# Kernel optimization log

Hardware: AMD Instinct MI355X
Metric: run time of the kernel (lower is better)

The kernel has to match this reference:

```python
import jax, jax.numpy as jnp
import numpy as np

B, S, HID = 2, 4096, 1024
H, D = 16, 64

def rotate_half(x):
    x1, x2 = jnp.split(x, 2, axis=-1)
    return jnp.concatenate([-x2, x1], axis=-1)

def setup_inputs() -> dict:
    key = jax.random.key(0)
    ks = jax.random.split(key, 8)
    hidden_states = jax.random.normal(ks[0], (B, S, HID), dtype=jnp.float32)
    pos = jnp.arange(S, dtype=jnp.float32)[:, None]
    inv_freq = 1.0 / (10000.0 ** (jnp.arange(0, D, 2, dtype=jnp.float32) / D))
    freqs = pos * inv_freq[None, :]
    emb = jnp.concatenate([freqs, freqs], axis=-1)  # [S, D]
    cos = jnp.cos(emb)
    sin = jnp.sin(emb)
    W_rkv = jax.random.normal(ks[1], (3 * H * D, HID), dtype=jnp.float32) * 0.02
    W_o = jax.random.normal(ks[2], (HID, H * D), dtype=jnp.float32) * 0.02
    # match torch init: uniform(-8,-5), uniform(-1,1), uniform(0.2,0.8)
    time_decay = jax.random.uniform(ks[3], (H, D), minval=-8.0, maxval=-5.0, dtype=jnp.float32)
    time_first = jax.random.uniform(ks[4], (H, D), minval=-1.0, maxval=1.0, dtype=jnp.float32)
    time_mix = jax.random.uniform(ks[5], (1, 1, HID), minval=0.2, maxval=0.8, dtype=jnp.float32)
    return {"hidden_states": hidden_states, "cos": cos, "sin": sin,
            "W_rkv": W_rkv, "W_o": W_o, "time_decay": time_decay,
            "time_first": time_first, "time_mix": time_mix}

def reference(hidden_states, cos, sin, W_rkv, W_o, time_decay, time_first, time_mix):
    b, s, hid = hidden_states.shape
    # token-shift time mixing
    xx = jnp.concatenate([jnp.zeros_like(hidden_states[:, :1]), hidden_states[:, :-1]], axis=1)
    mixed = hidden_states * time_mix + xx * (1.0 - time_mix)
    rkv = jnp.einsum('bsh,oh->bso', mixed, W_rkv).reshape(b, s, 3, H, D)
    r = jax.nn.sigmoid(rkv[:, :, 0])  # [B,S,H,D]
    k = rkv[:, :, 1]
    v = rkv[:, :, 2]
    # rotary on r, k
    c = cos[None, :, None, :]
    sn = sin[None, :, None, :]
    r = r * c + rotate_half(r) * sn
    k = k * c + rotate_half(k) * sn
    # fast rwkv linear attention (parallel approximation)
    w = -jnp.exp(time_decay)
    kv = k * v  # [B,S,H,D]
    pos = jnp.arange(s, dtype=hidden_states.dtype)
    pos_diff = pos[:, None] - pos[None, :]  # [S,S]
    mask = pos_diff > 0  # i > j masked (per original code)
    avg_decay = jnp.mean(w)
    pd = jnp.where(mask, 0.0, pos_diff)
    dw = jnp.where(mask, 0.0, jnp.exp(avg_decay * -jnp.abs(pd)))
    dw = dw / (dw.sum(axis=1, keepdims=True) + 1e-8)
    weighted_kv = jnp.einsum('ij,bjhd->bihd', dw, kv)
    out = r * (time_first[None, None] * kv + weighted_kv)  # [B,S,H,D]
    out = out.reshape(b, s, H * D)
    return jnp.einsum('bso,ho->bsh', out, W_o)
```

## Files before the change

### kernel.cpp

```cpp
#include <hip/hip_runtime.h>
#include <math.h>

#define S_LEN 4096
#define HIDN  1024
#define NH    16
#define HD    64
#define BATCH 2
#define M_TOTAL (BATCH * S_LEN)
#define N_RKV   (3 * HIDN)
#define CS 128
#define NC (S_LEN / CS)

typedef __attribute__((ext_vector_type(8))) _Float16 f16x8;
typedef __attribute__((ext_vector_type(4))) float f32x4;
typedef __attribute__((ext_vector_type(4))) unsigned short u16x4;

__device__ __forceinline__ unsigned short f2h(float x) {
    _Float16 h = (_Float16)x;
    return *(unsigned short*)&h;
}
__device__ __forceinline__ float h2f(unsigned short b) {
    _Float16 h = *(_Float16*)&b;
    return (float)h;
}

__device__ __forceinline__ void load_lds16(const void* g, void* l) {
    __builtin_amdgcn_global_load_lds((const __attribute__((address_space(1))) void*)g,
                                     (__attribute__((address_space(3))) void*)l, 16, 0, 0);
}

__global__ void k_avg_decay(const float* __restrict__ td, float* __restrict__ a_out) {
    int t = threadIdx.x;
    double acc = 0.0;
    for (int i = t; i < NH * HD; i += 64) acc += exp((double)td[i]);
    for (int off = 32; off > 0; off >>= 1) acc += __shfl_down(acc, off, 64);
    if (t == 0) a_out[0] = (float)(acc / (double)(NH * HD));
}

__global__ __launch_bounds__(256)
void k_split_mix(const float* __restrict__ hs, const float* __restrict__ tm,
                 unsigned short* __restrict__ Ah) {
    int g = blockIdx.x * 256 + threadIdx.x;
    int kc = (g & 255) * 4;
    int m = g >> 8;
    float4 cur = *(const float4*)&hs[(size_t)m * HIDN + kc];
    float4 t4  = *(const float4*)&tm[kc];
    float4 prev = make_float4(0.f, 0.f, 0.f, 0.f);
    if (m & (S_LEN - 1)) prev = *(const float4*)&hs[(size_t)(m - 1) * HIDN + kc];
    u16x4 h;
    h.x = f2h(cur.x * t4.x + prev.x * (1.f - t4.x));
    h.y = f2h(cur.y * t4.y + prev.y * (1.f - t4.y));
    h.z = f2h(cur.z * t4.z + prev.z * (1.f - t4.z));
    h.w = f2h(cur.w * t4.w + prev.w * (1.f - t4.w));
    *(u16x4*)&Ah[(size_t)m * HIDN + kc] = h;
}

__global__ __launch_bounds__(256)
void k_split_w(const float* __restrict__ W, unsigned short* __restrict__ Wh) {
    int g = blockIdx.x * 256 + threadIdx.x;
    size_t o = (size_t)g * 4;
    float4 v = *(const float4*)&W[o];
    u16x4 h;
    h.x = f2h(v.x); h.y = f2h(v.y); h.z = f2h(v.z); h.w = f2h(v.w);
    *(u16x4*)&Wh[o] = h;
}

__device__ __forceinline__ f32x4 mfma16(f16x8 a, f16x8 b, f32x4 c) {
    return __builtin_amdgcn_mfma_f32_16x16x32_f16(a, b, c, 0, 0, 0);
}

#define SBAR  do { __builtin_amdgcn_sched_barrier(0); __builtin_amdgcn_s_barrier(); \
                   __builtin_amdgcn_sched_barrier(0); } while (0)
#define LGKM0 do { asm volatile("s_waitcnt lgkmcnt(0)" ::: "memory"); \
                   __builtin_amdgcn_sched_barrier(0); } while (0)
#define VMC(n) asm volatile("s_waitcnt vmcnt(" #n ")" ::: "memory")

__global__ __launch_bounds__(512, 2)
void k_gemm1_8ph(const unsigned short* __restrict__ A,
                 const unsigned short* __restrict__ Bm,
                 unsigned short* __restrict__ C)
{
    __shared__ unsigned short smem[57344];
    const int tid  = threadIdx.x;
    const int lane = tid & 63;
    const int wv   = tid >> 6;
    const int wm = wv >> 2, wn = wv & 3;
    const int lm = lane & 15, rq = lane >> 4;
    const int swz = (lm & 7) << 4;

    const int cpx = gridDim.x >> 3;
    const int wg  = (blockIdx.x & 7) * cpx + (blockIdx.x >> 3);
    const int bx  = wg & 15;
    const int by  = wg >> 4;
    const int m0 = by * 256, n0 = bx * 192;

    const int srow = 8 * wv + (lane >> 3);
    const int scol = ((lane & 7) ^ (lane >> 3)) * 8;
    const unsigned short* sA = A  + (size_t)(m0 + srow) * 1024 + scol;
    const unsigned short* sB = Bm + (size_t)(n0 + srow) * 1024 + scol;
    unsigned short* dA = smem + wv * 512;
    unsigned short* dB = smem + 16384 + wv * 512;

#define STG_A(u, T, bf) load_lds16(sA + (u)*65536 + (T)*64, dA + (bf)*28672 + (u)*4096)
#define STG_B(u, T, bf) load_lds16(sB + (u)*65536 + (T)*64, dB + (bf)*28672 + (u)*4096)

    const int arow = (wm * 128 + lm) * 128 + rq * 16;
    int boff[3][2];
#pragma unroll
    for (int nt = 0; nt < 3; ++nt)
#pragma unroll
        for (int kk = 0; kk < 2; ++kk)
            boff[nt][kk] = (((wn * 48 + nt * 16 + lm) * 128 + rq * 16 + kk * 64) ^ swz);

    f16x8 aF[2][2], bF[3][2];
    f32x4 acc[8][3] = {};

#define READ_A(q, bf) { const char* Ab = (const char*)smem + (bf)*57344; \
    _Pragma("unroll") for (int m2 = 0; m2 < 2; ++m2) \
    _Pragma("unroll") for (int kk = 0; kk < 2; ++kk) \
        aF[m2][kk] = *(const f16x8*)(Ab + ((arow + (q)*4096 + m2*2048 + kk*64) ^ swz)); }

#define READ_B(bf) { const char* Bb = (const char*)smem + (bf)*57344 + 32768; \
    _Pragma("unroll") for (int nt = 0; nt < 3; ++nt) \
    _Pragma("unroll") for (int kk = 0; kk < 2; ++kk) \
        bF[nt][kk] = *(const f16x8*)(Bb + boff[nt][kk]); }

#define MMQ(q) { __builtin_amdgcn_s_setprio(1); \
    _Pragma("unroll") for (int kk = 0; kk < 2; ++kk) \
    _Pragma("unroll") for (int m2 = 0; m2 < 2; ++m2) \
    _Pragma("unroll") for (int nt = 0; nt < 3; ++nt) \
        acc[(q)*2+m2][nt] = mfma16(aF[m2][kk], bF[nt][kk], acc[(q)*2+m2][nt]); \
    __builtin_amdgcn_s_setprio(0); }

    STG_A(0,0,0); STG_A(1,0,0); STG_A(2,0,0); STG_A(3,0,0);
    STG_B(0,0,0); STG_B(1,0,0); STG_B(2,0,0);
    STG_B(0,1,1); STG_B(1,1,1); STG_B(2,1,1);
    STG_A(0,1,1); STG_A(2,1,1);
    VMC(5);
    SBAR;

    for (int it = 0; it < 8; ++it) {
        const int t = 2 * it;
        const bool st = (it < 7);
        READ_A(0, 0); READ_B(0);
        STG_A(1, t + 1, 1); STG_A(3, t + 1, 1);
        SBAR; LGKM0; MMQ(0); SBAR;
        READ_A(1, 0);
        if (st) { STG_B(0, t + 2, 0); STG_B(1, t + 2, 0); }
        SBAR; LGKM0; MMQ(1); SBAR;
        READ_A(2, 0);
        if (st) { STG_B(2, t + 2, 0); STG_A(0, t + 2, 0); }
        SBAR; LGKM0; MMQ(2); SBAR;
        READ_A(3, 0);
        if (st) { STG_A(2, t + 2, 0); }
        SBAR; LGKM0; MMQ(3);
        if (st) { VMC(5); } else { VMC(0); }
        SBAR;
        READ_A(0, 1); READ_B(1);
        if (st) { STG_A(1, t + 2, 0); STG_A(3, t + 2, 0); }
        SBAR; LGKM0; MMQ(0); SBAR;
        READ_A(1, 1);
        if (st) { STG_B(0, t + 3, 1); STG_B(1, t + 3, 1); }
        SBAR; LGKM0; MMQ(1); SBAR;
        READ_A(2, 1);
        if (st) { STG_B(2, t + 3, 1); STG_A(0, t + 3, 1); }
        SBAR; LGKM0; MMQ(2); SBAR;
        READ_A(3, 1);
        if (st) { STG_A(2, t + 3, 1); }
        SBAR; LGKM0; MMQ(3);
        if (st) { VMC(5); }
        SBAR;
    }

#pragma unroll
    for (int mt = 0; mt < 8; ++mt)
#pragma unroll
        for (int nt = 0; nt < 3; ++nt) {
            int col = n0 + wn * 48 + nt * 16 + lm;
#pragma unroll
            for (int r = 0; r < 4; ++r) {
                int row = m0 + wm * 128 + mt * 16 + rq * 4 + r;
                C[(size_t)row * N_RKV + col] = f2h(acc[mt][nt][r]);
            }
        }
}

template<int LDC, int NBX, bool HALF_OUT>
__global__ __launch_bounds__(256, 2)
void k_gemm_bt(const unsigned short* __restrict__ A,
               const unsigned short* __restrict__ Bm,
               void* __restrict__ Cv)
{
    __shared__ unsigned short smem[16384];
    const int tid  = threadIdx.x;
    const int lane = tid & 63;
    const int wave = tid >> 6;
    const int wm = wave >> 1, wn = wave & 1;

    const int cpx = gridDim.x >> 3;
    const int wg  = (blockIdx.x & 7) * cpx + (blockIdx.x >> 3);
    const int bx  = wg % NBX;
    const int by  = wg / NBX;
    const int m0 = by * 128;
    const int n0 = bx * 128;

    const unsigned short* segsrc[4];
    int segdst[4];
    {
        int rowoff = lane >> 2;
        int q = (lane & 3) ^ (rowoff & 3);
#pragma unroll
        for (int i = 0; i < 4; ++i) {
            int s = wave * 4 + i;
            const unsigned short* base = (s < 8) ? A : Bm;
            int row = (s < 8) ? (m0 + s * 16) : (n0 + (s - 8) * 16);
            segsrc[i] = base + (size_t)(row + rowoff) * 1024 + q * 8;
            segdst[i] = s * 512;
        }
    }

    const int lm = lane & 15;
    const int rq = lane >> 4;
    const int qx = rq ^ (lane & 3);
    int aoff[4], boff2[4];
#pragma unroll
    for (int t = 0; t < 4; ++t) {
        aoff[t]  = (wm * 64 + t * 16 + lm) * 32 + qx * 8;
        boff2[t] = 4096 + (wn * 64 + t * 16 + lm) * 32 + qx * 8;
    }

    f32x4 acc[4][4] = {};

#pragma unroll
    for (int i = 0; i < 4; ++i) load_lds16(segsrc[i], smem + segdst[i]);

    int p = 0;
    for (int kt = 0; kt < 1024; kt += 32) {
        __syncthreads();
        if (kt + 32 < 1024) {
#pragma unroll
            for (int i = 0; i < 4; ++i)
                load_lds16(segsrc[i] + kt + 32, smem + ((p ^ 1) * 8192 + segdst[i]));
        }
        const unsigned short* sb = smem + p * 8192;
        f16x8 fah[4], fb[4];
#pragma unroll
        for (int t = 0; t < 4; ++t) {
            fah[t] = *(const f16x8*)(sb + aoff[t]);
            fb[t]  = *(const f16x8*)(sb + boff2[t]);
        }
#pragma unroll
        for (int mt = 0; mt < 4; ++mt)
#pragma unroll
            for (int nt = 0; nt < 4; ++nt)
                acc[mt][nt] = mfma16(fah[mt], fb[nt], acc[mt][nt]);
        p ^= 1;
    }

#pragma unroll
    for (int mt = 0; mt < 4; ++mt)
#pragma unroll
        for (int nt = 0; nt < 4; ++nt) {
            int col = n0 + wn * 64 + nt * 16 + lm;
#pragma unroll
            for (int r = 0; r < 4; ++r) {
                int row = m0 + wm * 64 + mt * 16 + rq * 4 + r;
                if constexpr (HALF_OUT)
                    ((unsigned short*)Cv)[(size_t)row * LDC + col] = f2h(acc[mt][nt][r]);
                else
                    ((float*)Cv)[(size_t)row * LDC + col] = acc[mt][nt][r];
            }
        }
}

__global__ __launch_bounds__(256)
void k_cb(const unsigned short* __restrict__ rkv,
          const float* __restrict__ cosp, const float* __restrict__ sinp,
          const float* __restrict__ a_ptr, float* __restrict__ Cb)
{
    __shared__ float Ls[4][64][4];
    int bid = blockIdx.x;
    int c  = bid & (NC - 1);
    int bh = bid >> 5;
    int b = bh >> 4, h = bh & 15;
    int lane = threadIdx.x & 63;
    int wave = threadIdx.x >> 6;
    int lm = lane & 15;
    int rs = lane >> 4;
    int d0 = lm * 4;
    float a = a_ptr[0];
    float sgn = (lm < 8) ? -1.f : 1.f;
    float ps0 = 0.f, ps1 = 0.f, ps2 = 0.f, ps3 = 0.f;
#pragma unroll
    for (int it = 0; it < 8; ++it) {
        int t = wave * 32 + it * 4 + rs;
        int s = c * CS + t;
        const unsigned short* rk = rkv + ((size_t)b * S_LEN + s) * N_RKV + h * 64 + d0;
        u16x4 k4 = *(const u16x4*)(rk + 1024);
        u16x4 v4 = *(const u16x4*)(rk + 2048);
        float4 cs4 = *(const float4*)&cosp[s * HD + d0];
        float4 sn4 = *(const float4*)&sinp[s * HD + d0];
        float e = expf(a * (float)t);
        float k0 = h2f(k4.x), k1 = h2f(k4.y), k2 = h2f(k4.z), k3 = h2f(k4.w);
        float kp0 = __shfl_xor(k0, 8, 64);
        float kp1 = __shfl_xor(k1, 8, 64);
        float kp2 = __shfl_xor(k2, 8, 64);
        float kp3 = __shfl_xor(k3, 8, 64);
        ps0 += e * (k0 * cs4.x + sgn * kp0 * sn4.x) * h2f(v4.x);
        ps1 += e * (k1 * cs4.y + sgn * kp1 * sn4.y) * h2f(v4.y);
        ps2 += e * (k2 * cs4.z + sgn * kp2 * sn4.z) * h2f(v4.z);
        ps3 += e * (k3 * cs4.w + sgn * kp3 * sn4.w) * h2f(v4.w);
    }
    Ls[wave][lane][0] = ps0; Ls[wave][lane][1] = ps1;
    Ls[wave][lane][2] = ps2; Ls[wave][lane][3] = ps3;
    __syncthreads();
    if (threadIdx.x < 64) {
        int d = threadIdx.x;
        int lmm = d >> 2, j = d & 3;
        float sum = 0.f;
#pragma unroll
        for (int wvv = 0; wvv < 4; ++wvv)
#pragma unroll
            for (int r = 0; r < 4; ++r)
                sum += Ls[wvv][r * 16 + lmm][j];
        Cb[((size_t)bh * NC + c) * 64 + d] = sum;
    }
}

__global__ __launch_bounds__(64)
void k_chunk_suffix(const float* __restrict__ Cb, const float* __restrict__ a_ptr,
                    float* __restrict__ Sb) {
    int bh = blockIdx.x;
    int d = threadIdx.x;
    float a = a_ptr[0];
    float eaCS = expf(a * (float)CS);
    float run = 0.f;
    Sb[(size_t)(bh * NC + NC - 1) * 64 + d] = 0.f;
    for (int c = NC - 2; c >= 0; --c) {
        run = Cb[(size_t)(bh * NC + c + 1) * 64 + d] + eaCS * run;
        Sb[(size_t)(bh * NC + c) * 64 + d] = run;
    }
}

__global__ __launch_bounds__(256)
void k_ztab(const float* __restrict__ a_ptr, float* __restrict__ Zt) {
    int i = blockIdx.x * 256 + threadIdx.x;
    if (i < S_LEN) {
        float a = a_ptr[0];
        float em1a = expm1f(a);
        Zt[i] = 1.f / (expm1f(a * (float)(S_LEN - i)) / em1a + 1e-8f);
    }
}

__global__ __launch_bounds__(256)
void k_wkv2(const unsigned short* __restrict__ rkv,
            const float* __restrict__ cosp, const float* __restrict__ sinp,
            const float* __restrict__ Sb, const float* __restrict__ a_ptr,
            const float* __restrict__ tf, const float* __restrict__ Zt,
            unsigned short* __restrict__ outH) {
    __shared__ unsigned short L[3 * 128 * 64];
    __shared__ float Tl[4][64];
    int bid = blockIdx.x;
    int c  = bid & (NC - 1);
    int bh = bid >> 5;
    int b = bh >> 4, h = bh & 15;
    int lane = threadIdx.x & 63;
    int wave = threadIdx.x >> 6;
    int s0 = c * CS;

#pragma unroll
    for (int i = 0; i < 12; ++i) {
        int seg = wave * 12 + i;
        int stream = seg >> 4;
        int rg = seg & 15;
        int row = rg * 8 + (lane >> 3);
        const unsigned short* src = rkv
            + ((size_t)b * S_LEN + s0 + row) * N_RKV + stream * 1024 + h * 64
            + (lane & 7) * 8;
        load_lds16(src, L + stream * 8192 + rg * 512);
    }
    __syncthreads();

    float a = a_ptr[0];
    float ea = expf(a);
    const unsigned short* Lr = L;
    const unsigned short* Lk = L + 8192;
    const unsigned short* Lv = L + 16384;
    float sgn = (lane < 32) ? -1.f : 1.f;
    int lx = lane ^ 32;

    float kvreg[32], rreg[32];
    float w = 1.f, T = 0.f;
#pragma unroll
    for (int t = 0; t < 32; ++t) {
        int row = wave * 32 + t;
        float r_ = h2f(Lr[row * 64 + lane]);
        float k_ = h2f(Lk[row * 64 + lane]);
        float kp = h2f(Lk[row * 64 + lx]);
        float v_ = h2f(Lv[row * 64 + lane]);
        float cs = cosp[(s0 + row) * HD + lane];
        float sn = sinp[(s0 + row) * HD + lane];
        float sig = 1.f / (1.f + expf(-r_));
        float sigp = __shfl_xor(sig, 32, 64);
        rreg[t]  = sig * cs + sgn * sigp * sn;
        kvreg[t] = (k_ * cs + sgn * kp * sn) * v_;
        T += w * kvreg[t];
        w *= ea;
    }
    Tl[wave][lane] = T;
    __syncthreads();

    float e32 = expf(a * 32.f);
    float S_run = Sb[(size_t)bid * 64 + lane] * expf(a * 32.f * (float)(3 - wave));
    float f = 1.f;
    for (int wp = wave + 1; wp < 4; ++wp) {
        S_run += f * Tl[wp][lane];
        f *= e32;
    }
    float tfv = tf[h * HD + lane];
#pragma unroll
    for (int t = 31; t >= 0; --t) {
        float kv = kvreg[t];
        S_run = kv + ea * S_run;
        int ig = s0 + wave * 32 + t;
        float o = rreg[t] * (tfv * kv + S_run * Zt[ig]);
        size_t m = (size_t)b * S_LEN + ig;
        outH[m * HIDN + h * HD + lane] = f2h(o);
    }
}

extern "C" void kernel_launch(void* const* d_in, const int* in_sizes, int n_in,
                              void* d_out, int out_size, void* d_ws, size_t ws_size,
                              hipStream_t stream) {
    const float* hs    = (const float*)d_in[0];
    const float* cosp  = (const float*)d_in[1];
    const float* sinp  = (const float*)d_in[2];
    const float* W_rkv = (const float*)d_in[3];
    const float* W_o   = (const float*)d_in[4];
    const float* td    = (const float*)d_in[5];
    const float* tf    = (const float*)d_in[6];
    const float* tm    = (const float*)d_in[7];
    float* out = (float*)d_out;

    char* w = (char*)d_ws;
    unsigned short* rkvH = (unsigned short*)w;
    unsigned short* Ah   = (unsigned short*)(w + 50331648);
    unsigned short* outH = (unsigned short*)(w + 50331648);
    unsigned short* Wrh  = (unsigned short*)(w + 67108864);
    unsigned short* Woh  = (unsigned short*)(w + 73400320);
    float*          Cb   = (float*)(w + 75497472);
    float*          Sb   = (float*)(w + 75759616);
    float*          a_ptr= (float*)(w + 76021760);
    float*          Zt   = Cb;

    k_avg_decay<<<1, 64, 0, stream>>>(td, a_ptr);

    k_split_mix<<<(M_TOTAL * HIDN / 4) / 256, 256, 0, stream>>>(hs, tm, Ah);
    k_split_w<<<(N_RKV * HIDN / 4) / 256, 256, 0, stream>>>(W_rkv, Wrh);
    k_split_w<<<(HIDN * HIDN / 4) / 256, 256, 0, stream>>>(W_o, Woh);

    k_gemm1_8ph<<<512, 512, 0, stream>>>(Ah, Wrh, rkvH);

    k_cb<<<BATCH * NH * NC, 256, 0, stream>>>(rkvH, cosp, sinp, a_ptr, Cb);
    k_chunk_suffix<<<BATCH * NH, 64, 0, stream>>>(Cb, a_ptr, Sb);
    k_ztab<<<S_LEN / 256, 256, 0, stream>>>(a_ptr, Zt);
    k_wkv2<<<BATCH * NH * NC, 256, 0, stream>>>(rkvH, cosp, sinp, Sb, a_ptr, tf, Zt, outH);

    k_gemm_bt<HIDN, 8, false><<<512, 256, 0, stream>>>(outH, Woh, out);
}
```

Measured before the change: 232.6 us.

## Widen RKV GEMM tile to 256x384 with one block per CU

The first GEMM's block tile grows from 256x192 to 256x384, so each wave now holds 8x6 accumulator fragments. The grid is halved to 256 blocks, LDS per block rises to 160 KB, and launch bounds drop to one block per CU. The staging schedule is reworked to load six B sub-tiles per k-step and the wait counts are retuned. The aim is more MFMA work per LDS read and less global traffic per output, traded against lower occupancy and higher register pressure, with 256 blocks roughly matching the CU count as a single wave.

```diff
diff --git a/kernel.cpp b/kernel.cpp
--- a/kernel.cpp
+++ b/kernel.cpp
@@ -75,12 +75,12 @@
                    __builtin_amdgcn_sched_barrier(0); } while (0)
 #define VMC(n) asm volatile("s_waitcnt vmcnt(" #n ")" ::: "memory")
 
-__global__ __launch_bounds__(512, 2)
-void k_gemm1_8ph(const unsigned short* __restrict__ A,
-                 const unsigned short* __restrict__ Bm,
-                 unsigned short* __restrict__ C)
+__global__ __launch_bounds__(512, 1)
+void k_gemm1_wide(const unsigned short* __restrict__ A,
+                  const unsigned short* __restrict__ Bm,
+                  unsigned short* __restrict__ C)
 {
-    __shared__ unsigned short smem[57344];
+    __shared__ unsigned short smem[81920];
     const int tid  = threadIdx.x;
     const int lane = tid & 63;
     const int wv   = tid >> 6;
@@ -89,10 +89,10 @@
     const int swz = (lm & 7) << 4;
 
     const int cpx = gridDim.x >> 3;
-    const int wg  = (blockIdx.x & 7) * cpx + (blockIdx.x >> 3);
-    const int bx  = wg & 15;
-    const int by  = wg >> 4;
-    const int m0 = by * 256, n0 = bx * 192;
+    const int wg  = ((int)blockIdx.x & 7) * cpx + ((int)blockIdx.x >> 3);
+    const int bx  = wg & 7;
+    const int by  = wg >> 3;
+    const int m0 = by * 256, n0 = bx * 384;
 
     const int srow = 8 * wv + (lane >> 3);
     const int scol = ((lane & 7) ^ (lane >> 3)) * 8;
@@ -101,86 +101,88 @@
     unsigned short* dA = smem + wv * 512;
     unsigned short* dB = smem + 16384 + wv * 512;
 
-#define STG_A(u, T, bf) load_lds16(sA + (u)*65536 + (T)*64, dA + (bf)*28672 + (u)*4096)
-#define STG_B(u, T, bf) load_lds16(sB + (u)*65536 + (T)*64, dB + (bf)*28672 + (u)*4096)
+#define STG_A(u, T, bf) load_lds16(sA + (u)*65536 + (T)*64, dA + (bf)*40960 + (u)*4096)
+#define STG_B(u, T, bf) load_lds16(sB + (u)*65536 + (T)*64, dB + (bf)*40960 + (u)*4096)
 
     const int arow = (wm * 128 + lm) * 128 + rq * 16;
-    int boff[3][2];
-#pragma unroll
-    for (int nt = 0; nt < 3; ++nt)
+    int boff[6][2];
+#pragma unroll
+    for (int nt = 0; nt < 6; ++nt)
 #pragma unroll
         for (int kk = 0; kk < 2; ++kk)
-            boff[nt][kk] = (((wn * 48 + nt * 16 + lm) * 128 + rq * 16 + kk * 64) ^ swz);
-
-    f16x8 aF[2][2], bF[3][2];
-    f32x4 acc[8][3] = {};
-
-#define READ_A(q, bf) { const char* Ab = (const char*)smem + (bf)*57344; \
+            boff[nt][kk] = ((32768 + (wn * 96 + nt * 16 + lm) * 128 + rq * 16 + kk * 64) ^ swz);
+
+    f16x8 aF[2][2], bF[6][2];
+    f32x4 acc[8][6] = {};
+
+#define RDA(q, bf) { const char* Ab = (const char*)smem + (bf)*81920; \
     _Pragma("unroll") for (int m2 = 0; m2 < 2; ++m2) \
     _Pragma("unroll") for (int kk = 0; kk < 2; ++kk) \
         aF[m2][kk] = *(const f16x8*)(Ab + ((arow + (q)*4096 + m2*2048 + kk*64) ^ swz)); }
 
-#define READ_B(bf) { const char* Bb = (const char*)smem + (bf)*57344 + 32768; \
-    _Pragma("unroll") for (int nt = 0; nt < 3; ++nt) \
+#define RDB(bf) { const char* Bb = (const char*)smem + (bf)*81920; \
+    _Pragma("unroll") for (int nt = 0; nt < 6; ++nt) \
     _Pragma("unroll") for (int kk = 0; kk < 2; ++kk) \
         bF[nt][kk] = *(const f16x8*)(Bb + boff[nt][kk]); }
 
 #define MMQ(q) { __builtin_amdgcn_s_setprio(1); \
     _Pragma("unroll") for (int kk = 0; kk < 2; ++kk) \
     _Pragma("unroll") for (int m2 = 0; m2 < 2; ++m2) \
-    _Pragma("unroll") for (int nt = 0; nt < 3; ++nt) \
+    _Pragma("unroll") for (int nt = 0; nt < 6; ++nt) \
         acc[(q)*2+m2][nt] = mfma16(aF[m2][kk], bF[nt][kk], acc[(q)*2+m2][nt]); \
     __builtin_amdgcn_s_setprio(0); }
 
     STG_A(0,0,0); STG_A(1,0,0); STG_A(2,0,0); STG_A(3,0,0);
     STG_B(0,0,0); STG_B(1,0,0); STG_B(2,0,0);
+    STG_B(3,0,0); STG_B(4,0,0); STG_B(5,0,0);
     STG_B(0,1,1); STG_B(1,1,1); STG_B(2,1,1);
+    STG_B(3,1,1); STG_B(4,1,1); STG_B(5,1,1);
     STG_A(0,1,1); STG_A(2,1,1);
-    VMC(5);
+    VMC(8);
     SBAR;
 
     for (int it = 0; it < 8; ++it) {
         const int t = 2 * it;
-        const bool st = (it < 7);
-        READ_A(0, 0); READ_B(0);
+        const bool st = (t < 14);
+        RDA(0, 0); RDB(0);
         STG_A(1, t + 1, 1); STG_A(3, t + 1, 1);
         SBAR; LGKM0; MMQ(0); SBAR;
-        READ_A(1, 0);
-        if (st) { STG_B(0, t + 2, 0); STG_B(1, t + 2, 0); }
+        RDA(1, 0);
+        if (st) { STG_B(0, t + 2, 0); STG_B(1, t + 2, 0); STG_B(2, t + 2, 0); }
         SBAR; LGKM0; MMQ(1); SBAR;
-        READ_A(2, 0);
-        if (st) { STG_B(2, t + 2, 0); STG_A(0, t + 2, 0); }
+        RDA(2, 0);
+        if (st) { STG_B(3, t + 2, 0); STG_B(4, t + 2, 0); STG_B(5, t + 2, 0); }
         SBAR; LGKM0; MMQ(2); SBAR;
-        READ_A(3, 0);
-        if (st) { STG_A(2, t + 2, 0); }
+        RDA(3, 0);
+        if (st) { STG_A(0, t + 2, 0); STG_A(2, t + 2, 0); }
         SBAR; LGKM0; MMQ(3);
-        if (st) { VMC(5); } else { VMC(0); }
+        if (st) { VMC(8); } else { VMC(0); }
         SBAR;
-        READ_A(0, 1); READ_B(1);
+        RDA(0, 1); RDB(1);
         if (st) { STG_A(1, t + 2, 0); STG_A(3, t + 2, 0); }
         SBAR; LGKM0; MMQ(0); SBAR;
-        READ_A(1, 1);
-        if (st) { STG_B(0, t + 3, 1); STG_B(1, t + 3, 1); }
+        RDA(1, 1);
+        if (st) { STG_B(0, t + 3, 1); STG_B(1, t + 3, 1); STG_B(2, t + 3, 1); }
         SBAR; LGKM0; MMQ(1); SBAR;
-        READ_A(2, 1);
-        if (st) { STG_B(2, t + 3, 1); STG_A(0, t + 3, 1); }
+        RDA(2, 1);
+        if (st) { STG_B(3, t + 3, 1); STG_B(4, t + 3, 1); STG_B(5, t + 3, 1); }
         SBAR; LGKM0; MMQ(2); SBAR;
-        READ_A(3, 1);
-        if (st) { STG_A(2, t + 3, 1); }
+        RDA(3, 1);
+        if (st) { STG_A(0, t + 3, 1); STG_A(2, t + 3, 1); }
         SBAR; LGKM0; MMQ(3);
-        if (st) { VMC(5); }
+        if (st) { VMC(8); } else { VMC(0); }
         SBAR;
     }
 
 #pragma unroll
-    for (int mt = 0; mt < 8; ++mt)
-#pragma unroll
-        for (int nt = 0; nt < 3; ++nt) {
-            int col = n0 + wn * 48 + nt * 16 + lm;
+    for (int mf = 0; mf < 8; ++mf)
+#pragma unroll
+        for (int nf = 0; nf < 6; ++nf) {
+            int col = n0 + wn * 96 + nf * 16 + lm;
 #pragma unroll
             for (int r = 0; r < 4; ++r) {
-                int row = m0 + wm * 128 + mt * 16 + rq * 4 + r;
-                C[(size_t)row * N_RKV + col] = f2h(acc[mt][nt][r]);
+                int row = m0 + wm * 128 + mf * 16 + rq * 4 + r;
+                C[(size_t)row * N_RKV + col] = f2h(acc[mf][nf][r]);
             }
         }
 }
@@ -459,7 +461,7 @@
     k_split_w<<<(N_RKV * HIDN / 4) / 256, 256, 0, stream>>>(W_rkv, Wrh);
     k_split_w<<<(HIDN * HIDN / 4) / 256, 256, 0, stream>>>(W_o, Woh);
 
-    k_gemm1_8ph<<<512, 512, 0, stream>>>(Ah, Wrh, rkvH);
+    k_gemm1_wide<<<256, 512, 0, stream>>>(Ah, Wrh, rkvH);
 
     k_cb<<<BATCH * NH * NC, 256, 0, stream>>>(rkvH, cosp, sinp, a_ptr, Cb);
     k_chunk_suffix<<<BATCH * NH, 64, 0, stream>>>(Cb, a_ptr, Sb);
```

Result: slower. 374.2 us (+60.9%).
